# Kernel optimization log

Hardware: AMD Instinct MI355X
Metric: run time of the kernel (lower is better)

Reference implementation:

```python
import jax, jax.numpy as jnp
import numpy as np

N_NODES = 50000
N_EDGES = 800000
IN_DIM = 128
HIDDEN = 32
NHEAD = 4
OUT_DIM = 64
NEG_SLOPE = 0.2


def setup_inputs() -> dict:
    key = jax.random.key(0)
    ks = jax.random.split(key, 8)
    x = jax.random.normal(ks[0], (N_NODES, IN_DIM), dtype=jnp.float32)
    edge_index = jax.random.randint(ks[1], (2, N_EDGES), 0, N_NODES, dtype=jnp.int64)
    # layer 1: fc (in_dim -> nhead*hidden), attn [nhead, 2*hidden]
    W1 = jax.random.normal(ks[2], (IN_DIM, NHEAD * HIDDEN), dtype=jnp.float32) * 0.1
    attn1 = jax.random.normal(ks[3], (NHEAD, 2 * HIDDEN), dtype=jnp.float32) * 0.1
    # layer 2: fc (nhead*hidden -> 1*out_dim), attn [1, 2*out_dim]
    W2 = jax.random.normal(ks[4], (NHEAD * HIDDEN, OUT_DIM), dtype=jnp.float32) * 0.1
    attn2 = jax.random.normal(ks[5], (1, 2 * OUT_DIM), dtype=jnp.float32) * 0.1
    # extra output head: Linear(out_dim, out_dim) with bias
    head_W = jax.random.normal(ks[6], (OUT_DIM, OUT_DIM), dtype=jnp.float32) * 0.1
    head_b = jax.random.normal(ks[7], (OUT_DIM,), dtype=jnp.float32) * 0.1
    return {"x": x, "edge_index": edge_index, "W1": W1, "attn1": attn1,
            "W2": W2, "attn2": attn2, "head_W": head_W, "head_b": head_b}


def _gat_layer(x, W, attn, row, col, num_nodes, heads):
    """One GATConv: linear proj, edge attention, segment softmax over dst (col), scatter-add."""
    f_out = W.shape[1] // heads
    h = (x @ W).reshape(num_nodes, heads, f_out)            # [N, H, F]
    a_l, a_r = attn[:, :f_out], attn[:, f_out:]              # split attn for src/dst parts
    e_src = jnp.einsum('nhf,hf->nh', h, a_l)                 # [N, H]
    e_dst = jnp.einsum('nhf,hf->nh', h, a_r)                 # [N, H]
    alpha = e_src[row] + e_dst[col]                          # [E, H] == cat(h[row],h[col])·attn
    alpha = jax.nn.leaky_relu(alpha, NEG_SLOPE)
    # segment softmax grouped by destination node (col); self-loops guarantee non-empty segs
    amax = jax.ops.segment_max(alpha, col, num_segments=num_nodes)
    ex = jnp.exp(alpha - amax[col])
    denom = jax.ops.segment_sum(ex, col, num_segments=num_nodes)
    a = ex / denom[col]                                      # [E, H]
    msg = h[row] * a[:, :, None]                             # [E, H, F]
    out = jax.ops.segment_sum(msg, col, num_segments=num_nodes)  # [N, H, F]
    return out.reshape(num_nodes, heads * f_out)


def reference(x, edge_index, W1, attn1, W2, attn2, head_W, head_b):
    n = x.shape[0]
    loops = jnp.arange(n, dtype=edge_index.dtype)
    row = jnp.concatenate([edge_index[0], loops])
    col = jnp.concatenate([edge_index[1], loops])
    h = _gat_layer(x, W1, attn1, row, col, n, NHEAD)         # [N, NHEAD*HIDDEN]
    h = jax.nn.relu(h)                                       # intermediate-layer activation
    h = _gat_layer(h, W2, attn2, row, col, n, 1)             # [N, OUT_DIM] (last: no act)
    out = h @ head_W + head_b                                # extra_output_fc head
    return out
```

## Files before the change

### kernel.cpp

```cpp
#include <hip/hip_runtime.h>
#include <math.h>

#define N_NODES 50000
#define E_RAW 800000
#define E_TOT 850000
#define NEG_SLOPE 0.2f
#define G1_BLOCKS ((N_NODES + 63) / 64)
#define NBUCK 391
#define EPB 2048
#define PBLK ((E_TOT + EPB - 1) / EPB)

typedef __attribute__((ext_vector_type(8))) short bf16x8;
typedef __attribute__((ext_vector_type(4))) float f32x4;

__device__ __forceinline__ float lrelu(float a) { return a > 0.f ? a : NEG_SLOPE * a; }

__device__ __forceinline__ unsigned f2bf(float f) {
    unsigned u = __float_as_uint(f);
    return (u + 0x7fff + ((u >> 16) & 1)) >> 16;
}
__device__ __forceinline__ unsigned pack2(float a, float b) {
    return f2bf(a) | (f2bf(b) << 16);
}
__device__ __forceinline__ float bflo(unsigned p) { return __uint_as_float(p << 16); }
__device__ __forceinline__ float bfhi(unsigned p) { return __uint_as_float(p & 0xffff0000u); }

__global__ void k_prep(const float* __restrict__ W1, const float* __restrict__ W2,
                       unsigned* __restrict__ Btg, unsigned* __restrict__ B2tg) {
    int c = blockIdx.x;
    int tq = threadIdx.x;
    if (c < 128) {
        Btg[c * 64 + tq] = pack2(W1[(2 * tq) * 128 + c], W1[(2 * tq + 1) * 128 + c]);
    } else {
        int c2 = c - 128;
        B2tg[c2 * 64 + tq] = pack2(W2[(2 * tq) * 64 + c2], W2[(2 * tq + 1) * 64 + c2]);
    }
}

__global__ void k_gemm1_p1(const float* __restrict__ A, const unsigned* __restrict__ Btg,
                           const float* __restrict__ aux, uint2* __restrict__ C,
                           float* __restrict__ es, float* __restrict__ ed,
                           const int* __restrict__ ei, int* __restrict__ hist2d) {
    __shared__ unsigned As[64 * 64];
    if (blockIdx.x >= G1_BLOCKS) {
        int blk = blockIdx.x - G1_BLOCKS;
        int* h = (int*)As;
        for (int i = threadIdx.x; i < NBUCK; i += 256) h[i] = 0;
        __syncthreads();
        int base = blk * EPB;
        for (int i = threadIdx.x; i < EPB; i += 256) {
            int e = base + i;
            if (e >= E_TOT) break;
            int col = (e < E_RAW) ? ei[E_RAW + e] : (e - E_RAW);
            atomicAdd(&h[col >> 7], 1);
        }
        __syncthreads();
        for (int i = threadIdx.x; i < NBUCK; i += 256) hist2d[i * PBLK + blk] = h[i];
        return;
    }
    int t = threadIdx.x;
    int m0 = blockIdx.x * 64;
    int rows = min(64, N_NODES - m0);
    const float4* A4 = (const float4*)(A + (size_t)m0 * 128);
    for (int i = t; i < rows * 32; i += 256) {
        int row = i >> 5, k4 = i & 31;
        float4 v = A4[i];
        int byte = (k4 * 8) ^ ((row & 7) << 4);
        unsigned* p = &As[row * 64 + (byte >> 2)];
        p[0] = pack2(v.x, v.y);
        p[1] = pack2(v.z, v.w);
    }
    __syncthreads();
    int lane = t & 63, wave = t >> 6;
    int r15 = lane & 15, g = lane >> 4;
    int arow = wave * 16 + r15;
    f32x4 acc[8];
#pragma unroll
    for (int i = 0; i < 8; ++i) acc[i] = (f32x4){0.f, 0.f, 0.f, 0.f};
    const char* Abase = (const char*)As + arow * 256;
    int swz = (arow & 7) << 4;
    const char* Bbase = (const char*)Btg;
#pragma unroll
    for (int s = 0; s < 4; ++s) {
        bf16x8 xf = *(const bf16x8*)(Abase + ((64 * s + 16 * g) ^ swz));
#pragma unroll
        for (int tt = 0; tt < 8; ++tt) {
            bf16x8 wf = *(const bf16x8*)(Bbase + ((16 * tt + r15) * 256 + 64 * s + 16 * g));
            acc[tt] = __builtin_amdgcn_mfma_f32_16x16x32_bf16(wf, xf, acc[tt], 0, 0, 0);
        }
    }
    int grow = m0 + arow;
    bool valid = (arow < rows);
    if (valid) {
        uint2* C2 = C + (size_t)grow * 32;
#pragma unroll
        for (int tt = 0; tt < 8; ++tt) {
            uint2 v; v.x = pack2(acc[tt][0], acc[tt][1]); v.y = pack2(acc[tt][2], acc[tt][3]);
            C2[4 * tt + g] = v;
        }
    }
    float ps0 = 0.f, ps1 = 0.f, ps2 = 0.f, ps3 = 0.f;
    float pd0 = 0.f, pd1 = 0.f, pd2 = 0.f, pd3 = 0.f;
#pragma unroll
    for (int tt = 0; tt < 8; ++tt) {
        int h = tt >> 1;
        int fin = 16 * (tt & 1) + 4 * g;
        float4 alv = *(const float4*)(aux + h * 64 + fin);
        float4 arv = *(const float4*)(aux + h * 64 + 32 + fin);
        float s4 = acc[tt][0] * alv.x + acc[tt][1] * alv.y + acc[tt][2] * alv.z + acc[tt][3] * alv.w;
        float d4 = acc[tt][0] * arv.x + acc[tt][1] * arv.y + acc[tt][2] * arv.z + acc[tt][3] * arv.w;
        if (h == 0) { ps0 += s4; pd0 += d4; }
        else if (h == 1) { ps1 += s4; pd1 += d4; }
        else if (h == 2) { ps2 += s4; pd2 += d4; }
        else { ps3 += s4; pd3 += d4; }
    }
#pragma unroll
    for (int mask = 16; mask <= 32; mask <<= 1) {
        ps0 += __shfl_xor(ps0, mask); ps1 += __shfl_xor(ps1, mask);
        ps2 += __shfl_xor(ps2, mask); ps3 += __shfl_xor(ps3, mask);
        pd0 += __shfl_xor(pd0, mask); pd1 += __shfl_xor(pd1, mask);
        pd2 += __shfl_xor(pd2, mask); pd3 += __shfl_xor(pd3, mask);
    }
    if (valid) {
        float psg = (g == 0) ? ps0 : (g == 1) ? ps1 : (g == 2) ? ps2 : ps3;
        float pdg = (g == 0) ? pd0 : (g == 1) ? pd1 : (g == 2) ? pd2 : pd3;
        es[grow * 4 + g] = psg;
        ed[grow * 4 + g] = pdg;
    }
}

__global__ void k_p2a(const int* __restrict__ hist2d, int* __restrict__ off2d,
                      int* __restrict__ bucktot) {
    __shared__ int sh[512];
    int b = blockIdx.x, t = threadIdx.x;
    int v = (t < PBLK) ? hist2d[b * PBLK + t] : 0;
    sh[t] = v;
    __syncthreads();
    for (int ofs = 1; ofs < 512; ofs <<= 1) {
        int u = (t >= ofs) ? sh[t - ofs] : 0;
        __syncthreads();
        sh[t] += u;
        __syncthreads();
    }
    if (t < PBLK) off2d[b * PBLK + t] = sh[t] - v;
    if (t == 511) bucktot[b] = sh[511];
}

__global__ void k_p3(const int* __restrict__ ei, const int* __restrict__ off2d,
                     const int* __restrict__ bucktot, unsigned* __restrict__ part) {
    __shared__ int sh[512];
    __shared__ int h[NBUCK];
    __shared__ int basebuf[NBUCK];
    int blk = blockIdx.x, t = threadIdx.x;
    int v = (t < NBUCK) ? bucktot[t] : 0;
    sh[t] = v;
    if (t < NBUCK) h[t] = 0;
    __syncthreads();
    for (int ofs = 1; ofs < 512; ofs <<= 1) {
        int u = (t >= ofs) ? sh[t - ofs] : 0;
        __syncthreads();
        sh[t] += u;
        __syncthreads();
    }
    if (t < NBUCK) basebuf[t] = (sh[t] - v) + off2d[t * PBLK + blk];
    __syncthreads();
    int base = blk * EPB;
    for (int i = t; i < EPB; i += 512) {
        int e = base + i;
        if (e >= E_TOT) break;
        int col, src;
        if (e < E_RAW) { col = ei[E_RAW + e]; src = ei[e]; }
        else { col = src = e - E_RAW; }
        int b = col >> 7;
        int lr = atomicAdd(&h[b], 1);
        part[basebuf[b] + lr] = (unsigned)src | ((unsigned)(col & 127) << 16);
    }
}

__global__ void k_p4(const unsigned* __restrict__ part, const int* __restrict__ bucktot,
                     int* __restrict__ off, unsigned short* __restrict__ srcs) {
    __shared__ int sh[512];
    __shared__ int h[128];
    __shared__ int colofs[128];
    __shared__ int s0sh, s1sh;
    int b = blockIdx.x, t = threadIdx.x;
    int v = (t < NBUCK) ? bucktot[t] : 0;
    sh[t] = v;
    if (t < 128) h[t] = 0;
    __syncthreads();
    for (int ofs = 1; ofs < 512; ofs <<= 1) {
        int u = (t >= ofs) ? sh[t - ofs] : 0;
        __syncthreads();
        sh[t] += u;
        __syncthreads();
    }
    if (t == 0) { s1sh = sh[b]; s0sh = sh[b] - bucktot[b]; }
    __syncthreads();
    int s0 = s0sh, s1 = s1sh;
    for (int i = s0 + t; i < s1; i += 512) atomicAdd(&h[part[i] >> 16], 1);
    __syncthreads();
    if (t == 0) {
        int acc = 0;
        for (int c = 0; c < 128; ++c) { colofs[c] = acc; acc += h[c]; }
    }
    __syncthreads();
    int colbase = b * 128, ncols = min(128, N_NODES - colbase);
    if (t < ncols) off[colbase + t] = s0 + colofs[t];
    if (b == NBUCK - 1 && t == 0) off[N_NODES] = s1;
    if (t < 128) h[t] = colofs[t];
    __syncthreads();
    for (int i = s0 + t; i < s1; i += 512) {
        unsigned u = part[i];
        int c = u >> 16;
        int slot = atomicAdd(&h[c], 1);
        srcs[s0 + slot] = (unsigned short)(u & 0xffffu);
    }
}

__global__ void k_gemm2m(const unsigned* __restrict__ A, const unsigned* __restrict__ B2tg,
                         const float* __restrict__ aux, uint2* __restrict__ C,
                         float* __restrict__ es, float* __restrict__ ed) {
    __shared__ unsigned As[64 * 64];
    int t = threadIdx.x;
    int m0 = blockIdx.x * 64;
    int rows = min(64, N_NODES - m0);
    const uint4* A4 = (const uint4*)(A + (size_t)m0 * 64);
    for (int i = t; i < rows * 16; i += 256) {
        int row = i >> 4, q = i & 15;
        uint4 v = A4[i];
        int byte = (q * 16) ^ ((row & 7) << 4);
        unsigned* p = &As[row * 64 + (byte >> 2)];
        p[0] = v.x; p[1] = v.y; p[2] = v.z; p[3] = v.w;
    }
    __syncthreads();
    int lane = t & 63, wave = t >> 6;
    int r15 = lane & 15, g = lane >> 4;
    int arow = wave * 16 + r15;
    f32x4 acc[4];
#pragma unroll
    for (int i = 0; i < 4; ++i) acc[i] = (f32x4){0.f, 0.f, 0.f, 0.f};
    const char* Abase = (const char*)As + arow * 256;
    int swz = (arow & 7) << 4;
    const char* Bbase = (const char*)B2tg;
#pragma unroll
    for (int s = 0; s < 4; ++s) {
        bf16x8 xf = *(const bf16x8*)(Abase + ((64 * s + 16 * g) ^ swz));
#pragma unroll
        for (int tt = 0; tt < 4; ++tt) {
            bf16x8 wf = *(const bf16x8*)(Bbase + ((16 * tt + r15) * 256 + 64 * s + 16 * g));
            acc[tt] = __builtin_amdgcn_mfma_f32_16x16x32_bf16(wf, xf, acc[tt], 0, 0, 0);
        }
    }
    int grow = m0 + arow;
    bool valid = (arow < rows);
    if (valid) {
        uint2* C2 = C + (size_t)grow * 16;
#pragma unroll
        for (int tt = 0; tt < 4; ++tt) {
            uint2 v; v.x = pack2(acc[tt][0], acc[tt][1]); v.y = pack2(acc[tt][2], acc[tt][3]);
            C2[4 * tt + g] = v;
        }
    }
    float pl = 0.f, pr = 0.f;
#pragma unroll
    for (int tt = 0; tt < 4; ++tt) {
        int f0 = 16 * tt + 4 * g;
        float4 alv = *(const float4*)(aux + f0);
        float4 arv = *(const float4*)(aux + 64 + f0);
        pl += acc[tt][0] * alv.x + acc[tt][1] * alv.y + acc[tt][2] * alv.z + acc[tt][3] * alv.w;
        pr += acc[tt][0] * arv.x + acc[tt][1] * arv.y + acc[tt][2] * arv.z + acc[tt][3] * arv.w;
    }
#pragma unroll
    for (int mask = 16; mask <= 32; mask <<= 1) {
        pl += __shfl_xor(pl, mask);
        pr += __shfl_xor(pr, mask);
    }
    if (valid && g == 0) { es[grow] = pl; ed[grow] = pr; }
}

__global__ void k_agg1(const unsigned* __restrict__ h1b, const float* __restrict__ es,
                       const float* __restrict__ ed, const int* __restrict__ off,
                       const unsigned short* __restrict__ srcs, unsigned* __restrict__ out1) {
    int n = blockIdx.x * (blockDim.x >> 6) + (threadIdx.x >> 6);
    int lane = threadIdx.x & 63;
    if (n >= N_NODES) return;
    int myh = lane & 3;
    int jj = lane >> 2;
    float edh = ed[n * 4 + myh];
    int s = off[n], e = off[n + 1];
    int l16 = lane & 15;
    int esub = lane >> 4;
    int hcL = l16 >> 2;
    float acc[8];
#pragma unroll
    for (int i = 0; i < 8; ++i) acc[i] = 0.f;
    float psum = 0.f;
    for (int base = s; base < e; base += 16) {
        int cnt = e - base;
        int srcj = 0;
        float w = 0.f;
        if (jj < cnt) {
            srcj = srcs[base + jj];
            w = __expf(lrelu(es[srcj * 4 + myh] + edh));
        }
        psum += w;
        int src4[4];
        float wv4[4];
#pragma unroll
        for (int q = 0; q < 4; ++q) {
            int eidx = 4 * q + esub;
            src4[q] = __shfl(srcj, eidx * 4);
            wv4[q] = __shfl(w, eidx * 4 + hcL);
        }
        uint4 pv4[4];
#pragma unroll
        for (int q = 0; q < 4; ++q)
            pv4[q] = *((const uint4*)(h1b + (size_t)src4[q] * 64 + l16 * 4));
#pragma unroll
        for (int q = 0; q < 4; ++q) {
            float wv = wv4[q];
            acc[0] = fmaf(bflo(pv4[q].x), wv, acc[0]);
            acc[1] = fmaf(bfhi(pv4[q].x), wv, acc[1]);
            acc[2] = fmaf(bflo(pv4[q].y), wv, acc[2]);
            acc[3] = fmaf(bfhi(pv4[q].y), wv, acc[3]);
            acc[4] = fmaf(bflo(pv4[q].z), wv, acc[4]);
            acc[5] = fmaf(bfhi(pv4[q].z), wv, acc[5]);
            acc[6] = fmaf(bflo(pv4[q].w), wv, acc[6]);
            acc[7] = fmaf(bfhi(pv4[q].w), wv, acc[7]);
        }
    }
#pragma unroll
    for (int mask = 4; mask <= 32; mask <<= 1) psum += __shfl_xor(psum, mask);
    float inv = 1.f / __shfl(psum, hcL);
#pragma unroll
    for (int i = 0; i < 8; ++i) {
        acc[i] += __shfl_xor(acc[i], 16);
        acc[i] += __shfl_xor(acc[i], 32);
    }
    if (esub == 0) {
        uint4 o;
        o.x = pack2(fmaxf(acc[0] * inv, 0.f), fmaxf(acc[1] * inv, 0.f));
        o.y = pack2(fmaxf(acc[2] * inv, 0.f), fmaxf(acc[3] * inv, 0.f));
        o.z = pack2(fmaxf(acc[4] * inv, 0.f), fmaxf(acc[5] * inv, 0.f));
        o.w = pack2(fmaxf(acc[6] * inv, 0.f), fmaxf(acc[7] * inv, 0.f));
        *((uint4*)(out1 + (size_t)n * 64 + l16 * 4)) = o;
    }
}

__global__ void k_agg2h(const unsigned* __restrict__ h2b, const float* __restrict__ es,
                        const float* __restrict__ ed, const int* __restrict__ off,
                        const unsigned short* __restrict__ srcs,
                        const float* __restrict__ headW, const float* __restrict__ headb,
                        float* __restrict__ outv) {
    __shared__ float Wsh[64 * 64];
    __shared__ float rowsh[4][64];
    int t = threadIdx.x;
    {
        const float4* W4 = (const float4*)headW;
        float4* S4 = (float4*)Wsh;
        for (int i = t; i < 1024; i += 256) S4[i] = W4[i];
    }
    int wavei = t >> 6;
    int n = blockIdx.x * 4 + wavei;
    int lane = t & 63;
    float edv = ed[n];
    int s = off[n], e = off[n + 1];
    int l16 = lane & 15;
    int esub = lane >> 4;
    const uint2* gp = (const uint2*)h2b;
    float a0 = 0.f, a1 = 0.f, a2 = 0.f, a3 = 0.f, psum = 0.f;
    for (int base = s; base < e; base += 16) {
        int cnt = e - base;
        int srcj = 0;
        float w = 0.f;
        if (lane < 16 && lane < cnt) {
            srcj = srcs[base + lane];
            w = __expf(lrelu(es[srcj] + edv));
        }
        psum += w;
        int src4[4];
        float wv4[4];
#pragma unroll
        for (int q = 0; q < 4; ++q) {
            int eidx = 4 * q + esub;
            src4[q] = __shfl(srcj, eidx);
            wv4[q] = __shfl(w, eidx);
        }
        uint2 pv4[4];
#pragma unroll
        for (int q = 0; q < 4; ++q) pv4[q] = gp[(size_t)src4[q] * 16 + l16];
#pragma unroll
        for (int q = 0; q < 4; ++q) {
            a0 = fmaf(bflo(pv4[q].x), wv4[q], a0);
            a1 = fmaf(bfhi(pv4[q].x), wv4[q], a1);
            a2 = fmaf(bflo(pv4[q].y), wv4[q], a2);
            a3 = fmaf(bfhi(pv4[q].y), wv4[q], a3);
        }
    }
#pragma unroll
    for (int mask = 1; mask <= 8; mask <<= 1) psum += __shfl_xor(psum, mask);
    float inv = 1.f / __shfl(psum, 0);
    a0 += __shfl_xor(a0, 16); a0 += __shfl_xor(a0, 32);
    a1 += __shfl_xor(a1, 16); a1 += __shfl_xor(a1, 32);
    a2 += __shfl_xor(a2, 16); a2 += __shfl_xor(a2, 32);
    a3 += __shfl_xor(a3, 16); a3 += __shfl_xor(a3, 32);
    if (esub == 0) {
        rowsh[wavei][4 * l16 + 0] = a0 * inv;
        rowsh[wavei][4 * l16 + 1] = a1 * inv;
        rowsh[wavei][4 * l16 + 2] = a2 * inv;
        rowsh[wavei][4 * l16 + 3] = a3 * inv;
    }
    __syncthreads();
    float hacc = headb[lane];
#pragma unroll 8
    for (int k = 0; k < 64; ++k)
        hacc = fmaf(rowsh[wavei][k], Wsh[k * 64 + lane], hacc);
    outv[(size_t)n * 64 + lane] = hacc;
}

extern "C" void kernel_launch(void* const* d_in, const int* in_sizes, int n_in,
                              void* d_out, int out_size, void* d_ws, size_t ws_size,
                              hipStream_t stream) {
    const float* x     = (const float*)d_in[0];
    const int*   ei    = (const int*)d_in[1];
    const float* W1    = (const float*)d_in[2];
    const float* attn1 = (const float*)d_in[3];
    const float* W2    = (const float*)d_in[4];
    const float* attn2 = (const float*)d_in[5];
    const float* headW = (const float*)d_in[6];
    const float* headb = (const float*)d_in[7];
    float* out = (float*)d_out;

    char* ws = (char*)d_ws;
    size_t o = 0;
    auto alloc = [&](size_t bytes) -> void* {
        o = (o + 255) & ~(size_t)255;
        void* p = ws + o;
        o += bytes;
        return p;
    };
    unsigned*       h1b    = (unsigned*)alloc((size_t)N_NODES * 128 * 2);
    unsigned*       out1b  = (unsigned*)alloc((size_t)N_NODES * 128 * 2);
    unsigned*       h2b    = (unsigned*)alloc((size_t)N_NODES * 64 * 2);
    float*          e1s    = (float*)alloc((size_t)N_NODES * 4 * 4);
    float*          e1d    = (float*)alloc((size_t)N_NODES * 4 * 4);
    float*          e2s    = (float*)alloc((size_t)N_NODES * 4);
    float*          e2d    = (float*)alloc((size_t)N_NODES * 4);
    int*            off    = (int*)alloc((size_t)(N_NODES + 1) * 4);
    unsigned short* srcs   = (unsigned short*)alloc((size_t)E_TOT * 2);
    unsigned*       Btg    = (unsigned*)alloc((size_t)128 * 64 * 4);
    unsigned*       B2tg   = (unsigned*)alloc((size_t)64 * 64 * 4);
    int*            hist2d = (int*)alloc((size_t)NBUCK * PBLK * 4);
    int*            off2d  = (int*)alloc((size_t)NBUCK * PBLK * 4);
    int*            bucktot = (int*)alloc((size_t)NBUCK * 4);
    unsigned*       part   = (unsigned*)alloc((size_t)E_TOT * 4);

    k_prep<<<192, 64, 0, stream>>>(W1, W2, Btg, B2tg);

    k_gemm1_p1<<<G1_BLOCKS + PBLK, 256, 0, stream>>>(
        x, Btg, attn1, (uint2*)h1b, e1s, e1d, ei, hist2d);

    k_p2a<<<NBUCK, 512, 0, stream>>>(hist2d, off2d, bucktot);
    k_p3<<<PBLK, 512, 0, stream>>>(ei, off2d, bucktot, part);
    k_p4<<<NBUCK, 512, 0, stream>>>(part, bucktot, off, srcs);

    k_agg1<<<N_NODES / 4, 256, 0, stream>>>(h1b, e1s, e1d, off, srcs, out1b);

    k_gemm2m<<<(N_NODES + 63) / 64, 256, 0, stream>>>(out1b, B2tg, attn2, (uint2*)h2b, e2s, e2d);
    k_agg2h<<<N_NODES / 4, 256, 0, stream>>>(h2b, e2s, e2d, off, srcs, headW, headb, out);
}
```

Measured before the change: 219.5 us.

## Fold head linear into layer-2 weights and compute layer-2 attention scores in agg1

Precomputes W2·headW as a single combined weight, so the head matmul moves before the layer-2 aggregation (valid because the softmax weights sum to one, with the bias added afterwards). It also precomputes W2·attn2 vectors so the layer-2 source and destination scores come straight from the relu output inside agg1. This drops the per-node shared-memory head GEMM in the final kernel and the score reduction in the GEMM kernel. In exchange it adds a small prep kernel and changes rounding, since the head is now applied to bf16 pre-aggregation features.

```diff
diff --git a/kernel.cpp b/kernel.cpp
--- a/kernel.cpp
+++ b/kernel.cpp
@@ -25,15 +25,36 @@
 __device__ __forceinline__ float bflo(unsigned p) { return __uint_as_float(p << 16); }
 __device__ __forceinline__ float bfhi(unsigned p) { return __uint_as_float(p & 0xffff0000u); }
 
-__global__ void k_prep(const float* __restrict__ W1, const float* __restrict__ W2,
-                       unsigned* __restrict__ Btg, unsigned* __restrict__ B2tg) {
+__global__ void k_prep(const float* __restrict__ W1, unsigned* __restrict__ Btg) {
     int c = blockIdx.x;
     int tq = threadIdx.x;
-    if (c < 128) {
-        Btg[c * 64 + tq] = pack2(W1[(2 * tq) * 128 + c], W1[(2 * tq + 1) * 128 + c]);
+    Btg[c * 64 + tq] = pack2(W1[(2 * tq) * 128 + c], W1[(2 * tq + 1) * 128 + c]);
+}
+
+__global__ void k_prep2(const float* __restrict__ W2, const float* __restrict__ attn2,
+                        const float* __restrict__ headW,
+                        unsigned* __restrict__ Wctg, float* __restrict__ av) {
+    int b = blockIdx.x, t = threadIdx.x;
+    if (b < 64) {
+        if (t < 64) {
+            int f = b, q = t;
+            float s0 = 0.f, s1 = 0.f;
+            for (int j = 0; j < 64; ++j) {
+                float hw = headW[j * 64 + f];
+                s0 = fmaf(W2[(2 * q) * 64 + j], hw, s0);
+                s1 = fmaf(W2[(2 * q + 1) * 64 + j], hw, s1);
+            }
+            Wctg[f * 64 + q] = pack2(s0, s1);
+        }
     } else {
-        int c2 = c - 128;
-        B2tg[c2 * 64 + tq] = pack2(W2[(2 * tq) * 64 + c2], W2[(2 * tq + 1) * 64 + c2]);
+        int k = t;
+        float sl = 0.f, sr = 0.f;
+        for (int j = 0; j < 64; ++j) {
+            float w = W2[k * 64 + j];
+            sl = fmaf(w, attn2[j], sl);
+            sr = fmaf(w, attn2[64 + j], sr);
+        }
+        av[k] = sl; av[128 + k] = sr;
     }
 }
 
@@ -217,9 +238,8 @@
     }
 }
 
-__global__ void k_gemm2m(const unsigned* __restrict__ A, const unsigned* __restrict__ B2tg,
-                         const float* __restrict__ aux, uint2* __restrict__ C,
-                         float* __restrict__ es, float* __restrict__ ed) {
+__global__ void k_gemmv(const unsigned* __restrict__ A, const unsigned* __restrict__ Wctg,
+                        uint2* __restrict__ C) {
     __shared__ unsigned As[64 * 64];
     int t = threadIdx.x;
     int m0 = blockIdx.x * 64;
@@ -241,7 +261,7 @@
     for (int i = 0; i < 4; ++i) acc[i] = (f32x4){0.f, 0.f, 0.f, 0.f};
     const char* Abase = (const char*)As + arow * 256;
     int swz = (arow & 7) << 4;
-    const char* Bbase = (const char*)B2tg;
+    const char* Bbase = (const char*)Wctg;
 #pragma unroll
     for (int s = 0; s < 4; ++s) {
         bf16x8 xf = *(const bf16x8*)(Abase + ((64 * s + 16 * g) ^ swz));
@@ -252,8 +272,7 @@
         }
     }
     int grow = m0 + arow;
-    bool valid = (arow < rows);
-    if (valid) {
+    if (arow < rows) {
         uint2* C2 = C + (size_t)grow * 16;
 #pragma unroll
         for (int tt = 0; tt < 4; ++tt) {
@@ -261,26 +280,13 @@
             C2[4 * tt + g] = v;
         }
     }
-    float pl = 0.f, pr = 0.f;
-#pragma unroll
-    for (int tt = 0; tt < 4; ++tt) {
-        int f0 = 16 * tt + 4 * g;
-        float4 alv = *(const float4*)(aux + f0);
-        float4 arv = *(const float4*)(aux + 64 + f0);
-        pl += acc[tt][0] * alv.x + acc[tt][1] * alv.y + acc[tt][2] * alv.z + acc[tt][3] * alv.w;
-        pr += acc[tt][0] * arv.x + acc[tt][1] * arv.y + acc[tt][2] * arv.z + acc[tt][3] * arv.w;
-    }
-#pragma unroll
-    for (int mask = 16; mask <= 32; mask <<= 1) {
-        pl += __shfl_xor(pl, mask);
-        pr += __shfl_xor(pr, mask);
-    }
-    if (valid && g == 0) { es[grow] = pl; ed[grow] = pr; }
 }
 
 __global__ void k_agg1(const unsigned* __restrict__ h1b, const float* __restrict__ es,
                        const float* __restrict__ ed, const int* __restrict__ off,
-                       const unsigned short* __restrict__ srcs, unsigned* __restrict__ out1) {
+                       const unsigned short* __restrict__ srcs, const float* __restrict__ av,
+                       unsigned* __restrict__ out1,
+                       float* __restrict__ e2s, float* __restrict__ e2d) {
     int n = blockIdx.x * (blockDim.x >> 6) + (threadIdx.x >> 6);
     int lane = threadIdx.x & 63;
     if (n >= N_NODES) return;
@@ -337,37 +343,44 @@
         acc[i] += __shfl_xor(acc[i], 16);
         acc[i] += __shfl_xor(acc[i], 32);
     }
+    float o[8];
+#pragma unroll
+    for (int i = 0; i < 8; ++i) o[i] = fmaxf(acc[i] * inv, 0.f);
     if (esub == 0) {
-        uint4 o;
-        o.x = pack2(fmaxf(acc[0] * inv, 0.f), fmaxf(acc[1] * inv, 0.f));
-        o.y = pack2(fmaxf(acc[2] * inv, 0.f), fmaxf(acc[3] * inv, 0.f));
-        o.z = pack2(fmaxf(acc[4] * inv, 0.f), fmaxf(acc[5] * inv, 0.f));
-        o.w = pack2(fmaxf(acc[6] * inv, 0.f), fmaxf(acc[7] * inv, 0.f));
-        *((uint4*)(out1 + (size_t)n * 64 + l16 * 4)) = o;
-    }
-}
-
-__global__ void k_agg2h(const unsigned* __restrict__ h2b, const float* __restrict__ es,
+        uint4 ov;
+        ov.x = pack2(o[0], o[1]);
+        ov.y = pack2(o[2], o[3]);
+        ov.z = pack2(o[4], o[5]);
+        ov.w = pack2(o[6], o[7]);
+        *((uint4*)(out1 + (size_t)n * 64 + l16 * 4)) = ov;
+    }
+    float4 vl0 = *(const float4*)(av + 8 * l16);
+    float4 vl1 = *(const float4*)(av + 8 * l16 + 4);
+    float4 vr0 = *(const float4*)(av + 128 + 8 * l16);
+    float4 vr1 = *(const float4*)(av + 128 + 8 * l16 + 4);
+    float pl = o[0] * vl0.x + o[1] * vl0.y + o[2] * vl0.z + o[3] * vl0.w
+             + o[4] * vl1.x + o[5] * vl1.y + o[6] * vl1.z + o[7] * vl1.w;
+    float pr = o[0] * vr0.x + o[1] * vr0.y + o[2] * vr0.z + o[3] * vr0.w
+             + o[4] * vr1.x + o[5] * vr1.y + o[6] * vr1.z + o[7] * vr1.w;
+#pragma unroll
+    for (int mask = 1; mask <= 8; mask <<= 1) {
+        pl += __shfl_xor(pl, mask);
+        pr += __shfl_xor(pr, mask);
+    }
+    if (lane == 0) { e2s[n] = pl; e2d[n] = pr; }
+}
+
+__global__ void k_agg2f(const unsigned* __restrict__ v2b, const float* __restrict__ es,
                         const float* __restrict__ ed, const int* __restrict__ off,
                         const unsigned short* __restrict__ srcs,
-                        const float* __restrict__ headW, const float* __restrict__ headb,
-                        float* __restrict__ outv) {
-    __shared__ float Wsh[64 * 64];
-    __shared__ float rowsh[4][64];
-    int t = threadIdx.x;
-    {
-        const float4* W4 = (const float4*)headW;
-        float4* S4 = (float4*)Wsh;
-        for (int i = t; i < 1024; i += 256) S4[i] = W4[i];
-    }
-    int wavei = t >> 6;
-    int n = blockIdx.x * 4 + wavei;
-    int lane = t & 63;
+                        const float* __restrict__ headb, float* __restrict__ outv) {
+    int n = blockIdx.x * 4 + (threadIdx.x >> 6);
+    int lane = threadIdx.x & 63;
     float edv = ed[n];
     int s = off[n], e = off[n + 1];
     int l16 = lane & 15;
     int esub = lane >> 4;
-    const uint2* gp = (const uint2*)h2b;
+    const uint2* gp = (const uint2*)v2b;
     float a0 = 0.f, a1 = 0.f, a2 = 0.f, a3 = 0.f, psum = 0.f;
     for (int base = s; base < e; base += 16) {
         int cnt = e - base;
@@ -405,17 +418,14 @@
     a2 += __shfl_xor(a2, 16); a2 += __shfl_xor(a2, 32);
     a3 += __shfl_xor(a3, 16); a3 += __shfl_xor(a3, 32);
     if (esub == 0) {
-        rowsh[wavei][4 * l16 + 0] = a0 * inv;
-        rowsh[wavei][4 * l16 + 1] = a1 * inv;
-        rowsh[wavei][4 * l16 + 2] = a2 * inv;
-        rowsh[wavei][4 * l16 + 3] = a3 * inv;
-    }
-    __syncthreads();
-    float hacc = headb[lane];
-#pragma unroll 8
-    for (int k = 0; k < 64; ++k)
-        hacc = fmaf(rowsh[wavei][k], Wsh[k * 64 + lane], hacc);
-    outv[(size_t)n * 64 + lane] = hacc;
+        float4 bv = ((const float4*)headb)[l16];
+        float4 o;
+        o.x = fmaf(a0, inv, bv.x);
+        o.y = fmaf(a1, inv, bv.y);
+        o.z = fmaf(a2, inv, bv.z);
+        o.w = fmaf(a3, inv, bv.w);
+        ((float4*)outv)[(size_t)n * 16 + l16] = o;
+    }
 }
 
 extern "C" void kernel_launch(void* const* d_in, const int* in_sizes, int n_in,
@@ -441,7 +451,7 @@
     };
     unsigned*       h1b    = (unsigned*)alloc((size_t)N_NODES * 128 * 2);
     unsigned*       out1b  = (unsigned*)alloc((size_t)N_NODES * 128 * 2);
-    unsigned*       h2b    = (unsigned*)alloc((size_t)N_NODES * 64 * 2);
+    unsigned*       v2b    = (unsigned*)alloc((size_t)N_NODES * 64 * 2);
     float*          e1s    = (float*)alloc((size_t)N_NODES * 4 * 4);
     float*          e1d    = (float*)alloc((size_t)N_NODES * 4 * 4);
     float*          e2s    = (float*)alloc((size_t)N_NODES * 4);
@@ -449,13 +459,15 @@
     int*            off    = (int*)alloc((size_t)(N_NODES + 1) * 4);
     unsigned short* srcs   = (unsigned short*)alloc((size_t)E_TOT * 2);
     unsigned*       Btg    = (unsigned*)alloc((size_t)128 * 64 * 4);
-    unsigned*       B2tg   = (unsigned*)alloc((size_t)64 * 64 * 4);
+    unsigned*       Wctg   = (unsigned*)alloc((size_t)64 * 64 * 4);
+    float*          av     = (float*)alloc((size_t)256 * 4);
     int*            hist2d = (int*)alloc((size_t)NBUCK * PBLK * 4);
     int*            off2d  = (int*)alloc((size_t)NBUCK * PBLK * 4);
     int*            bucktot = (int*)alloc((size_t)NBUCK * 4);
     unsigned*       part   = (unsigned*)alloc((size_t)E_TOT * 4);
 
-    k_prep<<<192, 64, 0, stream>>>(W1, W2, Btg, B2tg);
+    k_prep<<<128, 64, 0, stream>>>(W1, Btg);
+    k_prep2<<<65, 128, 0, stream>>>(W2, attn2, headW, Wctg, av);
 
     k_gemm1_p1<<<G1_BLOCKS + PBLK, 256, 0, stream>>>(
         x, Btg, attn1, (uint2*)h1b, e1s, e1d, ei, hist2d);
@@ -464,8 +476,9 @@
     k_p3<<<PBLK, 512, 0, stream>>>(ei, off2d, bucktot, part);
     k_p4<<<NBUCK, 512, 0, stream>>>(part, bucktot, off, srcs);
 
-    k_agg1<<<N_NODES / 4, 256, 0, stream>>>(h1b, e1s, e1d, off, srcs, out1b);
-
-    k_gemm2m<<<(N_NODES + 63) / 64, 256, 0, stream>>>(out1b, B2tg, attn2, (uint2*)h2b, e2s, e2d);
-    k_agg2h<<<N_NODES / 4, 256, 0, stream>>>(h2b, e2s, e2d, off, srcs, headW, headb, out);
-}
+    k_agg1<<<N_NODES / 4, 256, 0, stream>>>(h1b, e1s, e1d, off, srcs, av, out1b, e2s, e2d);
+
+    k_gemmv<<<(N_NODES + 63) / 64, 256, 0, stream>>>(out1b, Wctg, (uint2*)v2b);
+
+    k_agg2f<<<N_NODES / 4, 256, 0, stream>>>(v2b, e2s, e2d, off, srcs, headb, out);
+}
```

New measurement: 209.4 us. 4.6% less time.
